# Performance work log

Hardware: AMD Instinct MI355X
Metric: run time of the kernel (lower is better)

The kernel has to match this reference:

```python
import jax, jax.numpy as jnp
import numpy as np

STRIDES = (8, 16, 32)
FMP = ((160, 160), (80, 80), (40, 40))
NUM_CLASSES = 80
TOPK = 1000
CONF_THRESH = 0.05
NMS_THRESH = 0.6
IMG_MAX = 1280.0
CLASS_OFFSET = 8192.0  # > any box coordinate, separates classes for batched NMS


def setup_inputs() -> dict:
    key = jax.random.key(0)
    ks = jax.random.split(key, 32)
    C = 256
    inp = {}
    for l, (h, w) in enumerate(FMP):
        inp[f'feat{l}'] = jax.random.normal(ks[l], (1, C, h, w), dtype=jnp.float32)
        inp[f'Wobj{l}'] = jax.random.normal(ks[3 + 6 * l + 0], (1, C), dtype=jnp.float32) * 0.05
        inp[f'bobj{l}'] = jnp.zeros((1,), dtype=jnp.float32)
        inp[f'Wcls{l}'] = jax.random.normal(ks[3 + 6 * l + 2], (NUM_CLASSES, C), dtype=jnp.float32) * 0.05
        inp[f'bcls{l}'] = jnp.zeros((NUM_CLASSES,), dtype=jnp.float32)
        inp[f'Wreg{l}'] = jax.random.normal(ks[3 + 6 * l + 4], (4, C), dtype=jnp.float32) * 0.05
        inp[f'breg{l}'] = jnp.zeros((4,), dtype=jnp.float32)
    return inp


def _level(feat, Wo, bo, Wc, bc, Wr, br, stride):
    x = feat[0]  # [C,H,W]
    H, W = x.shape[1], x.shape[2]
    def conv1x1(Wm, bv):
        # 1x1 conv == channel GEMM; output [H*W, O]
        return (jnp.einsum('oc,chw->hwo', Wm, x) + bv).reshape(H * W, -1)
    obj = conv1x1(Wo, bo)              # [M,1]
    cls = conv1x1(Wc, bc)              # [M,C]
    reg = jnp.exp(conv1x1(Wr, br)) * stride  # [M,4] (l,t,r,b)
    prob = jax.nn.sigmoid(obj) * jax.nn.sigmoid(cls)
    scores = prob.max(axis=-1)
    labels = prob.argmax(axis=-1)
    ay, ax = jnp.meshgrid(jnp.arange(H), jnp.arange(W), indexing='ij')
    anchors = (jnp.stack([ax, ay], axis=-1).astype(jnp.float32).reshape(-1, 2) + 0.5) * stride
    k = min(TOPK, H * W)
    scores, idx = jax.lax.top_k(scores, k)
    labels = labels[idx]
    reg = reg[idx]
    anchors = anchors[idx]
    boxes = jnp.concatenate([anchors - reg[:, :2], anchors + reg[:, 2:]], axis=-1)
    return scores, labels, boxes


def _batched_nms(boxes, scores, labels):
    N = boxes.shape[0]
    valid = scores >= CONF_THRESH
    # class-offset trick: per-class NMS == single NMS on disjoint offset boxes
    ob = boxes + labels.astype(boxes.dtype)[:, None] * CLASS_OFFSET
    order = jnp.argsort(-scores)
    b = ob[order]
    v = valid[order]
    x1, y1, x2, y2 = b[:, 0], b[:, 1], b[:, 2], b[:, 3]
    areas = (x2 - x1) * (y2 - y1)
    xx1 = jnp.maximum(x1[:, None], x1[None, :])
    yy1 = jnp.maximum(y1[:, None], y1[None, :])
    xx2 = jnp.minimum(x2[:, None], x2[None, :])
    yy2 = jnp.minimum(y2[:, None], y2[None, :])
    w = jnp.maximum(1e-10, xx2 - xx1)
    h = jnp.maximum(1e-10, yy2 - yy1)
    inter = w * h
    iou = inter / (areas[:, None] + areas[None, :] - inter + 1e-14)
    idxs = jnp.arange(N)
    def body(i, keep):
        sup = keep[i] & (iou[i] > NMS_THRESH) & (idxs > i)
        return keep & ~sup
    keep_sorted = jax.lax.fori_loop(0, N, body, v)
    keep = jnp.zeros(N, dtype=bool).at[order].set(keep_sorted)
    return keep


def reference(feat0, feat1, feat2,
              Wobj0, bobj0, Wcls0, bcls0, Wreg0, breg0,
              Wobj1, bobj1, Wcls1, bcls1, Wreg1, breg1,
              Wobj2, bobj2, Wcls2, bcls2, Wreg2, breg2):
    feats = (feat0, feat1, feat2)
    params = ((Wobj0, bobj0, Wcls0, bcls0, Wreg0, breg0),
              (Wobj1, bobj1, Wcls1, bcls1, Wreg1, breg1),
              (Wobj2, bobj2, Wcls2, bcls2, Wreg2, breg2))
    ss, ll, bb = [], [], []
    for l in range(3):
        s, lab, box = _level(feats[l], *params[l], STRIDES[l])
        ss.append(s); ll.append(lab); bb.append(box)
    scores = jnp.concatenate(ss)
    labels = jnp.concatenate(ll)
    boxes = jnp.concatenate(bb)
    keep = _batched_nms(boxes, scores, labels)
    bboxes = jnp.clip(boxes / IMG_MAX, 0.0, 1.0)
    return bboxes, scores, labels.astype(jnp.int32), keep
```

## Files before the change

### kernel.cpp

```cpp
#include <hip/hip_runtime.h>
#include <math.h>

#define NTOT   33600
#define NSEL   3000
#define CAND_CAP 8192
#define NWORDS 47
#define NROWS_PAD 3008
#define FCAP 4
#define NGRP 525
#define WPER 21760
#define NCH 17
#define NSLC 16

struct P21 {
  const float* feat[3];
  const float* Wobj[3];
  const float* bobj[3];
  const float* Wcls[3];
  const float* bcls[3];
  const float* Wreg[3];
  const float* breg[3];
};

__device__ __forceinline__ void level_of_block128(int b, int t, int& l, int& p, int& g,
                                                  int& HW, int& Wd, double& stride) {
  if (b < 200)      { l = 0; p = b * 128 + t;         g = p;          HW = 25600; Wd = 160; stride = 8.0;  }
  else if (b < 250) { l = 1; p = (b - 200) * 128 + t; g = 25600 + p;  HW = 6400;  Wd = 80;  stride = 16.0; }
  else              { l = 2; p = (b - 250) * 128 + t; g = 32000 + p;  HW = 1600;  Wd = 40;  stride = 32.0; }
}

__device__ __forceinline__ void level_of_group(int grp, int lane, int& l, int& p, int& g,
                                               int& HW, int& Wd, double& stride) {
  if (grp < 400)      { l = 0; p = grp * 64 + lane;         g = p;         HW = 25600; Wd = 160; stride = 8.0;  }
  else if (grp < 500) { l = 1; p = (grp - 400) * 64 + lane; g = 25600 + p; HW = 6400;  Wd = 80;  stride = 16.0; }
  else                { l = 2; p = (grp - 500) * 64 + lane; g = 32000 + p; HW = 1600;  Wd = 40;  stride = 32.0; }
}

__device__ __forceinline__ double sigmoid_d(double x) { return 1.0 / (1.0 + exp(-x)); }

__device__ __forceinline__ unsigned long long shfl64(unsigned long long v, int src) {
  unsigned lo = (unsigned)__shfl((int)(unsigned)(v & 0xFFFFFFFFull), src, 64);
  unsigned hi = (unsigned)__shfl((int)(unsigned)(v >> 32), src, 64);
  return (((unsigned long long)hi) << 32) | (unsigned long long)lo;
}

__global__ __launch_bounds__(256) void k_wconv(P21 P, double* __restrict__ W64) {
  int id = blockIdx.x * 256 + threadIdx.x;
  if (id >= 3 * WPER) return;
  int l = id / WPER, r = id - l * WPER;
  const float* src;
  if (r < 256)        src = P.Wobj[l] + r;
  else if (r < 1280)  src = P.Wreg[l] + (r - 256);
  else                src = P.Wcls[l] + (r - 1280);
  W64[id] = (double)(*src);
}

__global__ __launch_bounds__(128) void k_conv_chunk(P21 P, const double* __restrict__ W64,
    double* __restrict__ obj_t, double* __restrict__ reg_t,
    double* __restrict__ cmax, int* __restrict__ clab) {
  int l, p, g, HW, Wd; double stride;
  level_of_block128(blockIdx.x, threadIdx.x, l, p, g, HW, Wd, stride);
  if (p >= HW) return;
  const int ch = blockIdx.y;
  const float* __restrict__ fp = P.feat[l] + p;
  const double* __restrict__ Wl = W64 + l * WPER;

  if (ch == 0) {
    const double* __restrict__ Wo = Wl;
    const double* __restrict__ Wr = Wl + 256;
    double accO = (double)P.bobj[l][0];
    double accR[4];
#pragma unroll
    for (int j = 0; j < 4; j++) accR[j] = (double)P.breg[l][j];
    for (int c = 0; c < 256; c += 8) {
      double xc[8];
#pragma unroll
      for (int u = 0; u < 8; u++) xc[u] = (double)fp[(c + u) * HW];
#pragma unroll
      for (int u = 0; u < 8; u++) {
        accO = fma(Wo[c + u], xc[u], accO);
#pragma unroll
        for (int j = 0; j < 4; j++)
          accR[j] = fma(Wr[j * 256 + c + u], xc[u], accR[j]);
      }
    }
    obj_t[g] = accO;
#pragma unroll
    for (int j = 0; j < 4; j++) reg_t[4 * g + j] = accR[j];
  } else {
    const int base = (ch - 1) * 5;
    const double* __restrict__ Wc = Wl + 1280 + base * 256;
    const float* __restrict__ bcls = P.bcls[l];
    double a[5];
#pragma unroll
    for (int j = 0; j < 5; j++) a[j] = (double)bcls[base + j];
    for (int c = 0; c < 256; c += 8) {
      double xc[8];
#pragma unroll
      for (int u = 0; u < 8; u++) xc[u] = (double)fp[(c + u) * HW];
#pragma unroll
      for (int u = 0; u < 8; u++) {
#pragma unroll
        for (int j = 0; j < 5; j++)
          a[j] = fma(Wc[j * 256 + c + u], xc[u], a[j]);
      }
    }
    double maxv = a[0]; int lab = base;
#pragma unroll
    for (int j = 1; j < 5; j++) if (a[j] > maxv) { maxv = a[j]; lab = base + j; }
    cmax[(ch - 1) * NTOT + g] = maxv;
    clab[(ch - 1) * NTOT + g] = lab;
  }
}

__global__ __launch_bounds__(64) void k_combine(
    const double* __restrict__ obj_t, const double* __restrict__ reg_t,
    const double* __restrict__ cmax, const int* __restrict__ clab,
    double* __restrict__ score_d, int* __restrict__ label_d,
    double* __restrict__ box_d, unsigned* __restrict__ hist) {
  int l, p, g, HW, Wd; double stride;
  level_of_group(blockIdx.x, threadIdx.x, l, p, g, HW, Wd, stride);

  double maxv = cmax[g]; int lab = clab[g];
#pragma unroll
  for (int k = 1; k < NSLC; k++) {
    double v = cmax[k * NTOT + g];
    int lb = clab[k * NTOT + g];
    if (v > maxv) { maxv = v; lab = lb; }
  }
  double score = sigmoid_d(obj_t[g]) * sigmoid_d(maxv);
  int h = p / Wd, w = p - h * Wd;
  double ax = ((double)w + 0.5) * stride;
  double ay = ((double)h + 0.5) * stride;
  double e0 = exp(reg_t[4 * g + 0]) * stride;
  double e1 = exp(reg_t[4 * g + 1]) * stride;
  double e2 = exp(reg_t[4 * g + 2]) * stride;
  double e3 = exp(reg_t[4 * g + 3]) * stride;

  score_d[g] = score;
  label_d[g] = lab;
  box_d[4 * g + 0] = ax - e0;
  box_d[4 * g + 1] = ay - e1;
  box_d[4 * g + 2] = ax + e2;
  box_d[4 * g + 3] = ay + e3;

  unsigned key = __float_as_uint((float)score);
  atomicAdd(&hist[l * 65536 + (key >> 16)], 1u);
}

__global__ __launch_bounds__(256) void k_scan_a(const unsigned* __restrict__ hist,
                                                unsigned* __restrict__ csG) {
  const int lane = threadIdx.x & 63;
  const int row = blockIdx.x * 4 + (threadIdx.x >> 6);
  const uint4* hp = (const uint4*)(hist + row * 256);
  uint4 v = hp[lane];
  unsigned s = v.x + v.y + v.z + v.w;
#pragma unroll
  for (int off = 32; off > 0; off >>= 1) s += (unsigned)__shfl_down((int)s, off, 64);
  if (lane == 0) csG[row] = s;
}

__global__ __launch_bounds__(256) void k_scan_b(const unsigned* __restrict__ hist,
                                                const unsigned* __restrict__ csG,
                                                unsigned* __restrict__ cutB) {
  int l = blockIdx.x;
  __shared__ unsigned cs[256];
  __shared__ unsigned hb[256];
  __shared__ int s_chunk;
  __shared__ unsigned s_acc;
  int t = threadIdx.x;
  cs[t] = csG[l * 256 + t];
  __syncthreads();
  if (t == 0) {
    unsigned acc = 0; int chunk = 0;
    for (int tt = 255; tt >= 0; tt--) {
      if (acc + cs[tt] >= 1000u) { chunk = tt; break; }
      acc += cs[tt];
    }
    s_chunk = chunk; s_acc = acc;
  }
  __syncthreads();
  int chunk = s_chunk;
  hb[t] = hist[l * 65536 + chunk * 256 + t];
  __syncthreads();
  if (t == 0) {
    unsigned acc = s_acc;
    unsigned B = (unsigned)(chunk * 256);
    for (int b = 255; b >= 0; b--) {
      unsigned c = hb[b];
      if (acc + c >= 1000u) { B = (unsigned)(chunk * 256 + b); break; }
      acc += c;
    }
    cutB[l] = B;
  }
}

__global__ __launch_bounds__(64) void k_compact(const double* __restrict__ score_d,
    const unsigned* __restrict__ cutB, unsigned* __restrict__ cnt,
    double* __restrict__ cand_s, int* __restrict__ cand_g) {
  int l, p, g, HW, Wd; double stride;
  level_of_group(blockIdx.x, threadIdx.x, l, p, g, HW, Wd, stride);
  double sc = score_d[g];
  unsigned key = __float_as_uint((float)sc);
  if ((key >> 16) >= cutB[l]) {
    unsigned pos = atomicAdd(&cnt[l], 1u);
    if (pos < CAND_CAP) {
      cand_s[l * CAND_CAP + pos] = sc;
      cand_g[l * CAND_CAP + pos] = g;
    }
  }
}

__global__ __launch_bounds__(256) void k_rank(const double* __restrict__ cand_s,
    const int* __restrict__ cand_g, const unsigned* __restrict__ cnt,
    const int* __restrict__ label_d, const double* __restrict__ box_d,
    double* __restrict__ sel_s, int* __restrict__ sel_lab, double* __restrict__ sel_box) {
  const int l = blockIdx.y;
  const int M = (int)min(cnt[l], (unsigned)CAND_CAP);
  if (blockIdx.x * 4 >= M) return;
  const int q = blockIdx.x * 4 + (threadIdx.x >> 6);
  const int lane = threadIdx.x & 63;
  const bool active = (q < M);

  double s = 0.0; int g = 0;
  if (active) { s = cand_s[l * CAND_CAP + q]; g = cand_g[l * CAND_CAP + q]; }

  int r = 0;
  if (active) {
    for (int j = lane; j < M; j += 64) {
      double sj = cand_s[l * CAND_CAP + j];
      int gj = cand_g[l * CAND_CAP + j];
      r += (sj > s) || (sj == s && gj < g);
    }
  }
#pragma unroll
  for (int off = 32; off > 0; off >>= 1) r += __shfl_down(r, off, 64);

  if (active && lane == 0 && r < 1000) {
    int o = l * 1000 + r;
    sel_s[o] = s;
    sel_lab[o] = label_d[g];
    sel_box[4 * o + 0] = box_d[4 * g + 0];
    sel_box[4 * o + 1] = box_d[4 * g + 1];
    sel_box[4 * o + 2] = box_d[4 * g + 2];
    sel_box[4 * o + 3] = box_d[4 * g + 3];
  }
}

__global__ __launch_bounds__(256) void k_order(const double* __restrict__ sel_s,
                                               int* __restrict__ sortIdx) {
  const int i = blockIdx.x;
  const int t = threadIdx.x;
  const double s = sel_s[i];
  int r = 0;
  for (int j = t; j < NSEL; j += 256) {
    double sj = sel_s[j];
    r += (sj > s) || (sj == s && j < i);
  }
#pragma unroll
  for (int off = 32; off > 0; off >>= 1) r += __shfl_down(r, off, 64);
  __shared__ int wsum[4];
  if ((t & 63) == 0) wsum[t >> 6] = r;
  __syncthreads();
  if (t == 0) sortIdx[wsum[0] + wsum[1] + wsum[2] + wsum[3]] = i;
}

__global__ __launch_bounds__(256) void k_build(const double* __restrict__ sel_s,
    const int* __restrict__ sel_lab, const double* __restrict__ sel_box,
    const int* __restrict__ sortIdx, double* __restrict__ sbox, int* __restrict__ svalid) {
  int r = blockIdx.x * 256 + threadIdx.x;
  if (r >= NSEL) return;
  int i = sortIdx[r];
  double off = (double)sel_lab[i] * 8192.0;
  sbox[4 * r + 0] = sel_box[4 * i + 0] + off;
  sbox[4 * r + 1] = sel_box[4 * i + 1] + off;
  sbox[4 * r + 2] = sel_box[4 * i + 2] + off;
  sbox[4 * r + 3] = sel_box[4 * i + 3] + off;
  svalid[r] = (sel_s[i] >= 0.05) ? 1 : 0;
}

__global__ __launch_bounds__(256) void k_mask(const double* __restrict__ sbox,
    unsigned long long* __restrict__ denseG, unsigned long long* __restrict__ diagG,
    unsigned short* __restrict__ entG, int* __restrict__ cntGi) {
  const int w = blockIdx.x;
  const int rc = blockIdx.y;
  const int t = threadIdx.x, lane = t & 63, wk = t >> 6;
  const int rbase = rc * 64;
  if (w < rc) {
    int i = rbase + t;
    if (t < 64 && i < NSEL) denseG[(size_t)i * 48 + w] = 0ull;
    return;
  }
  __shared__ double rbox[256];
  {
    int idx = rbase * 4 + t;
    rbox[t] = (idx < NSEL * 4) ? sbox[idx] : 0.0;
  }
  const int j = w * 64 + lane;
  const bool jok = (j < NSEL);
  double bx1 = 0, by1 = 0, bx2 = 0, by2 = 0, arj = 0;
  if (jok) {
    bx1 = sbox[4 * j + 0]; by1 = sbox[4 * j + 1];
    bx2 = sbox[4 * j + 2]; by2 = sbox[4 * j + 3];
    arj = (bx2 - bx1) * (by2 - by1);
  }
  __syncthreads();
#pragma unroll
  for (int rr = 0; rr < 16; rr++) {
    const int ro = wk * 16 + rr;
    const int i = rbase + ro;
    if (i >= NSEL) break;
    double x1 = rbox[ro * 4 + 0], y1 = rbox[ro * 4 + 1];
    double x2 = rbox[ro * 4 + 2], y2 = rbox[ro * 4 + 3];
    double ar = (x2 - x1) * (y2 - y1);
    bool c = false;
    if (jok && j > i) {
      double xx1 = fmax(x1, bx1), yy1 = fmax(y1, by1);
      double xx2 = fmin(x2, bx2), yy2 = fmin(y2, by2);
      double ww = fmax(1e-10, xx2 - xx1);
      double hh = fmax(1e-10, yy2 - yy1);
      double inter = ww * hh;
      double iou = inter / (ar + arj - inter + 1e-14);
      c = iou > 0.6;
    }
    unsigned long long word = __ballot(c);
    if (lane == 0) {
      denseG[(size_t)i * 48 + w] = word;
      if (w == rc) diagG[i] = word;
      else if (word) {
        unsigned long long tt = word;
        while (tt) {
          int b = __builtin_ctzll(tt); tt &= tt - 1;
          int slot = atomicAdd(&cntGi[i], 1);
          if (slot < FCAP) entG[i * FCAP + slot] = (unsigned short)(w * 64 + b);
        }
      }
    }
  }
}

__global__ __launch_bounds__(256) void k_nms_scan(
    const unsigned long long* __restrict__ denseG, const unsigned long long* __restrict__ diagG,
    const unsigned short* __restrict__ entG, const int* __restrict__ cntGi,
    const int* __restrict__ svalid, const int* __restrict__ sortIdx,
    int* __restrict__ keepOrig) {
  __shared__ unsigned long long diagL[NROWS_PAD];
  __shared__ unsigned short entL[NROWS_PAD * FCAP];
  __shared__ unsigned short cntL[NROWS_PAD];
  __shared__ unsigned long long validL[48];
  __shared__ unsigned long long hasWL[48];
  const int t = threadIdx.x;
  const int lane = t & 63;

  for (int k = t; k < NSEL; k += 256) diagL[k] = diagG[k];
  for (int k = NSEL + t; k < NROWS_PAD; k += 256) diagL[k] = 0ull;
  uint2* e2 = (uint2*)entL; const uint2* eg2 = (const uint2*)entG;
  for (int k = t; k < NSEL; k += 256) e2[k] = eg2[k];
  for (int k = NSEL + t; k < NROWS_PAD; k += 256) { uint2 z; z.x = 0; z.y = 0; e2[k] = z; }
  for (int k = t; k < NSEL; k += 256) cntL[k] = (unsigned short)cntGi[k];
  for (int k = NSEL + t; k < NROWS_PAD; k += 256) cntL[k] = 0;
  for (int i0 = t; i0 < NROWS_PAD; i0 += 256) {
    bool f = (i0 < NSEL) && (svalid[i0] != 0);
    unsigned long long b = __ballot(f);
    if ((t & 63) == 0) validL[i0 >> 6] = b;
  }
  __syncthreads();
  if (t >= 64) return;

  for (int w = 0; w < NWORDS; w++) {
    int i = w * 64 + lane;
    bool f = (diagL[i] != 0ull) || (cntL[i] != 0);
    unsigned long long b = __ballot(f);
    if (lane == 0) hasWL[w] = b;
  }

  unsigned long long rem = 0ull;
  unsigned long long keep = 0ull;
  for (int w = 0; w < NWORDS; w++) {
    unsigned long long vw = validL[w];
    unsigned long long remw = shfl64(rem, w);
    unsigned long long win = vw & ~remw;
    unsigned long long work = hasWL[w];
    while (work) {
      int d = __builtin_ctzll(work); work &= work - 1;
      if ((win >> d) & 1ull) {
        int i = w * 64 + d;
        win &= ~diagL[i];
        int c = cntL[i];
        if (c > FCAP) {
          unsigned long long rowj = (lane < NWORDS) ? denseG[(size_t)i * 48 + lane] : 0ull;
          rem |= rowj;
        } else {
          for (int k = 0; k < c; k++) {
            int j = entL[i * FCAP + k];
            if ((j >> 6) == lane) rem |= 1ull << (j & 63);
          }
        }
      }
    }
    if (lane == w) keep = win;
  }
  if (lane < NWORDS) {
    for (int b = 0; b < 64; b++) {
      int j = lane * 64 + b;
      if (j < NSEL) keepOrig[sortIdx[j]] = (int)((keep >> b) & 1ull);
    }
  }
}

__global__ __launch_bounds__(256) void k_out(const double* __restrict__ sel_s,
    const int* __restrict__ sel_lab, const double* __restrict__ sel_box,
    const int* __restrict__ keepOrig, float* __restrict__ out) {
  int i = blockIdx.x * 256 + threadIdx.x;
  if (i >= NSEL) return;
#pragma unroll
  for (int c = 0; c < 4; c++) {
    double v = sel_box[4 * i + c] / 1280.0;
    v = fmin(fmax(v, 0.0), 1.0);
    out[4 * i + c] = (float)v;
  }
  out[12000 + i] = (float)sel_s[i];
  out[15000 + i] = (float)sel_lab[i];
  out[18000 + i] = keepOrig[i] ? 1.0f : 0.0f;
}

extern "C" void kernel_launch(void* const* d_in, const int* in_sizes, int n_in,
                              void* d_out, int out_size, void* d_ws, size_t ws_size,
                              hipStream_t stream) {
  P21 P;
  for (int l = 0; l < 3; l++) {
    P.feat[l] = (const float*)d_in[7 * l + 0];
    P.Wobj[l] = (const float*)d_in[7 * l + 1];
    P.bobj[l] = (const float*)d_in[7 * l + 2];
    P.Wcls[l] = (const float*)d_in[7 * l + 3];
    P.bcls[l] = (const float*)d_in[7 * l + 4];
    P.Wreg[l] = (const float*)d_in[7 * l + 5];
    P.breg[l] = (const float*)d_in[7 * l + 6];
  }

  char* ws = (char*)d_ws;
  size_t off = 0;
  auto alloc = [&](size_t bytes) -> char* {
    char* p = ws + off;
    off += (bytes + 15) & ~(size_t)15;
    return p;
  };
  double* score_d  = (double*)alloc((size_t)NTOT * 8);
  double* box_d    = (double*)alloc((size_t)NTOT * 4 * 8);
  int*    label_d  = (int*)   alloc((size_t)NTOT * 4);
  double* obj_t    = (double*)alloc((size_t)NTOT * 8);
  double* reg_t    = (double*)alloc((size_t)NTOT * 4 * 8);
  double* cmax     = (double*)alloc((size_t)NSLC * NTOT * 8);
  int*    clab     = (int*)   alloc((size_t)NSLC * NTOT * 4);
  double* W64      = (double*)alloc((size_t)3 * WPER * 8);
  double* sel_s    = (double*)alloc((size_t)NSEL * 8);
  double* sel_box  = (double*)alloc((size_t)NSEL * 4 * 8);
  int*    sel_lab  = (int*)   alloc((size_t)NSEL * 4);
  int*    sortIdx  = (int*)   alloc((size_t)NSEL * 4);
  double* sbox     = (double*)alloc((size_t)NSEL * 4 * 8);
  int*    svalid   = (int*)   alloc((size_t)NSEL * 4);
  int*    keepOrig = (int*)   alloc((size_t)NSEL * 4);
  double* cand_s   = (double*)alloc((size_t)3 * CAND_CAP * 8);
  int*    cand_g   = (int*)   alloc((size_t)3 * CAND_CAP * 4);
  unsigned long long* denseG = (unsigned long long*)alloc((size_t)NSEL * 48 * 8);
  unsigned long long* diagG  = (unsigned long long*)alloc((size_t)NSEL * 8);
  unsigned short*     entG   = (unsigned short*)alloc((size_t)NSEL * FCAP * 2);
  unsigned* hist   = (unsigned*)alloc((size_t)3 * 65536 * 4);
  unsigned* cnt    = (unsigned*)alloc(16);
  int*      cntGi  = (int*)   alloc((size_t)NSEL * 4);
  unsigned* cutB   = (unsigned*)alloc(16);
  unsigned* csG    = (unsigned*)alloc((size_t)768 * 4);

  hipMemsetAsync(hist, 0, (size_t)3 * 65536 * 4 + 16 + (size_t)NSEL * 4, stream);

  k_wconv   <<<(3 * WPER + 255) / 256, 256, 0, stream>>>(P, W64);
  dim3 cgrid(263, NCH, 1);
  k_conv_chunk<<<cgrid, 128, 0, stream>>>(P, W64, obj_t, reg_t, cmax, clab);
  k_combine <<<NGRP, 64, 0, stream>>>(obj_t, reg_t, cmax, clab, score_d, label_d, box_d, hist);
  k_scan_a  <<<192, 256, 0, stream>>>(hist, csG);
  k_scan_b  <<<3, 256, 0, stream>>>(hist, csG, cutB);
  k_compact <<<NGRP, 64, 0, stream>>>(score_d, cutB, cnt, cand_s, cand_g);
  dim3 rgrid(CAND_CAP / 4, 3, 1);
  k_rank    <<<rgrid, 256, 0, stream>>>(cand_s, cand_g, cnt, label_d, box_d,
                                        sel_s, sel_lab, sel_box);
  k_order   <<<NSEL, 256, 0, stream>>>(sel_s, sortIdx);
  k_build   <<<(NSEL + 255) / 256, 256, 0, stream>>>(sel_s, sel_lab, sel_box, sortIdx, sbox, svalid);
  dim3 mgrid(NWORDS, NWORDS, 1);
  k_mask    <<<mgrid, 256, 0, stream>>>(sbox, denseG, diagG, entG, cntGi);
  k_nms_scan<<<1, 256, 0, stream>>>(denseG, diagG, entG, cntGi, svalid, sortIdx, keepOrig);
  k_out     <<<(NSEL + 255) / 256, 256, 0, stream>>>(sel_s, sel_lab, sel_box, keepOrig, (float*)d_out);
}
```

Baseline: 307.0 us.

## Register-block conv over two pixels and eight classes, fuse build into order, triangular mask grid

The 1x1-conv kernel now computes two adjacent pixels per thread with float2 loads and eight classes per chunk instead of five, which halves the block count and reuses each fp64 weight load across two pixels. The k_build kernel is folded into k_order so the sorted boxes are written directly. The mask kernel launches only the upper-triangular tiles, and the lower tiles are zeroed by a memset. This trades higher register pressure in the conv for fewer weight loads and fewer launches, and adds a small serial loop per mask block to decode its tile index.

```diff
diff --git a/kernel.cpp b/kernel.cpp
--- a/kernel.cpp
+++ b/kernel.cpp
@@ -9,8 +9,8 @@
 #define FCAP 4
 #define NGRP 525
 #define WPER 21760
-#define NCH 17
-#define NSLC 16
+#define NSLC 10
+#define NTRI 1128
 
 struct P21 {
   const float* feat[3];
@@ -22,13 +22,6 @@
   const float* breg[3];
 };
 
-__device__ __forceinline__ void level_of_block128(int b, int t, int& l, int& p, int& g,
-                                                  int& HW, int& Wd, double& stride) {
-  if (b < 200)      { l = 0; p = b * 128 + t;         g = p;          HW = 25600; Wd = 160; stride = 8.0;  }
-  else if (b < 250) { l = 1; p = (b - 200) * 128 + t; g = 25600 + p;  HW = 6400;  Wd = 80;  stride = 16.0; }
-  else              { l = 2; p = (b - 250) * 128 + t; g = 32000 + p;  HW = 1600;  Wd = 40;  stride = 32.0; }
-}
-
 __device__ __forceinline__ void level_of_group(int grp, int lane, int& l, int& p, int& g,
                                                int& HW, int& Wd, double& stride) {
   if (grp < 400)      { l = 0; p = grp * 64 + lane;         g = p;         HW = 25600; Wd = 160; stride = 8.0;  }
@@ -58,8 +51,11 @@
 __global__ __launch_bounds__(128) void k_conv_chunk(P21 P, const double* __restrict__ W64,
     double* __restrict__ obj_t, double* __restrict__ reg_t,
     double* __restrict__ cmax, int* __restrict__ clab) {
-  int l, p, g, HW, Wd; double stride;
-  level_of_block128(blockIdx.x, threadIdx.x, l, p, g, HW, Wd, stride);
+  const int b = blockIdx.x, t = threadIdx.x;
+  int l, p, g, HW;
+  if (b < 100)      { l = 0; p = b * 256 + 2 * t;         g = p;         HW = 25600; }
+  else if (b < 125) { l = 1; p = (b - 100) * 256 + 2 * t; g = 25600 + p; HW = 6400;  }
+  else              { l = 2; p = (b - 125) * 256 + 2 * t; g = 32000 + p; HW = 1600;  }
   if (p >= HW) return;
   const int ch = blockIdx.y;
   const float* __restrict__ fp = P.feat[l] + p;
@@ -68,48 +64,62 @@
   if (ch == 0) {
     const double* __restrict__ Wo = Wl;
     const double* __restrict__ Wr = Wl + 256;
-    double accO = (double)P.bobj[l][0];
-    double accR[4];
-#pragma unroll
-    for (int j = 0; j < 4; j++) accR[j] = (double)P.breg[l][j];
+    double o0 = (double)P.bobj[l][0], o1 = o0;
+    double r0[4], r1[4];
+#pragma unroll
+    for (int j = 0; j < 4; j++) { r0[j] = (double)P.breg[l][j]; r1[j] = r0[j]; }
     for (int c = 0; c < 256; c += 8) {
-      double xc[8];
-#pragma unroll
-      for (int u = 0; u < 8; u++) xc[u] = (double)fp[(c + u) * HW];
+      double x0[8], x1[8];
 #pragma unroll
       for (int u = 0; u < 8; u++) {
-        accO = fma(Wo[c + u], xc[u], accO);
-#pragma unroll
-        for (int j = 0; j < 4; j++)
-          accR[j] = fma(Wr[j * 256 + c + u], xc[u], accR[j]);
-      }
-    }
-    obj_t[g] = accO;
-#pragma unroll
-    for (int j = 0; j < 4; j++) reg_t[4 * g + j] = accR[j];
+        float2 v = *(const float2*)(fp + (c + u) * HW);
+        x0[u] = (double)v.x; x1[u] = (double)v.y;
+      }
+#pragma unroll
+      for (int u = 0; u < 8; u++) {
+        double w = Wo[c + u];
+        o0 = fma(w, x0[u], o0); o1 = fma(w, x1[u], o1);
+#pragma unroll
+        for (int j = 0; j < 4; j++) {
+          double wr = Wr[j * 256 + c + u];
+          r0[j] = fma(wr, x0[u], r0[j]); r1[j] = fma(wr, x1[u], r1[j]);
+        }
+      }
+    }
+    obj_t[g] = o0; obj_t[g + 1] = o1;
+#pragma unroll
+    for (int j = 0; j < 4; j++) { reg_t[4 * g + j] = r0[j]; reg_t[4 * g + 4 + j] = r1[j]; }
   } else {
-    const int base = (ch - 1) * 5;
+    const int base = (ch - 1) * 8;
     const double* __restrict__ Wc = Wl + 1280 + base * 256;
     const float* __restrict__ bcls = P.bcls[l];
-    double a[5];
-#pragma unroll
-    for (int j = 0; j < 5; j++) a[j] = (double)bcls[base + j];
+    double a0[8], a1[8];
+#pragma unroll
+    for (int j = 0; j < 8; j++) { a0[j] = (double)bcls[base + j]; a1[j] = a0[j]; }
     for (int c = 0; c < 256; c += 8) {
-      double xc[8];
-#pragma unroll
-      for (int u = 0; u < 8; u++) xc[u] = (double)fp[(c + u) * HW];
+      double x0[8], x1[8];
 #pragma unroll
       for (int u = 0; u < 8; u++) {
-#pragma unroll
-        for (int j = 0; j < 5; j++)
-          a[j] = fma(Wc[j * 256 + c + u], xc[u], a[j]);
-      }
-    }
-    double maxv = a[0]; int lab = base;
-#pragma unroll
-    for (int j = 1; j < 5; j++) if (a[j] > maxv) { maxv = a[j]; lab = base + j; }
-    cmax[(ch - 1) * NTOT + g] = maxv;
-    clab[(ch - 1) * NTOT + g] = lab;
+        float2 v = *(const float2*)(fp + (c + u) * HW);
+        x0[u] = (double)v.x; x1[u] = (double)v.y;
+      }
+#pragma unroll
+      for (int u = 0; u < 8; u++) {
+#pragma unroll
+        for (int j = 0; j < 8; j++) {
+          double w = Wc[j * 256 + c + u];
+          a0[j] = fma(w, x0[u], a0[j]); a1[j] = fma(w, x1[u], a1[j]);
+        }
+      }
+    }
+    double m0 = a0[0], m1 = a1[0]; int l0 = base, l1 = base;
+#pragma unroll
+    for (int j = 1; j < 8; j++) {
+      if (a0[j] > m0) { m0 = a0[j]; l0 = base + j; }
+      if (a1[j] > m1) { m1 = a1[j]; l1 = base + j; }
+    }
+    cmax[(ch - 1) * NTOT + g] = m0; cmax[(ch - 1) * NTOT + g + 1] = m1;
+    clab[(ch - 1) * NTOT + g] = l0; clab[(ch - 1) * NTOT + g + 1] = l1;
   }
 }
 
@@ -248,7 +258,8 @@
 }
 
 __global__ __launch_bounds__(256) void k_order(const double* __restrict__ sel_s,
-                                               int* __restrict__ sortIdx) {
+    const int* __restrict__ sel_lab, const double* __restrict__ sel_box,
+    int* __restrict__ sortIdx, double* __restrict__ sbox, int* __restrict__ svalid) {
   const int i = blockIdx.x;
   const int t = threadIdx.x;
   const double s = sel_s[i];
@@ -262,35 +273,26 @@
   __shared__ int wsum[4];
   if ((t & 63) == 0) wsum[t >> 6] = r;
   __syncthreads();
-  if (t == 0) sortIdx[wsum[0] + wsum[1] + wsum[2] + wsum[3]] = i;
-}
-
-__global__ __launch_bounds__(256) void k_build(const double* __restrict__ sel_s,
-    const int* __restrict__ sel_lab, const double* __restrict__ sel_box,
-    const int* __restrict__ sortIdx, double* __restrict__ sbox, int* __restrict__ svalid) {
-  int r = blockIdx.x * 256 + threadIdx.x;
-  if (r >= NSEL) return;
-  int i = sortIdx[r];
-  double off = (double)sel_lab[i] * 8192.0;
-  sbox[4 * r + 0] = sel_box[4 * i + 0] + off;
-  sbox[4 * r + 1] = sel_box[4 * i + 1] + off;
-  sbox[4 * r + 2] = sel_box[4 * i + 2] + off;
-  sbox[4 * r + 3] = sel_box[4 * i + 3] + off;
-  svalid[r] = (sel_s[i] >= 0.05) ? 1 : 0;
+  if (t == 0) {
+    int rr = wsum[0] + wsum[1] + wsum[2] + wsum[3];
+    sortIdx[rr] = i;
+    double off = (double)sel_lab[i] * 8192.0;
+    sbox[4 * rr + 0] = sel_box[4 * i + 0] + off;
+    sbox[4 * rr + 1] = sel_box[4 * i + 1] + off;
+    sbox[4 * rr + 2] = sel_box[4 * i + 2] + off;
+    sbox[4 * rr + 3] = sel_box[4 * i + 3] + off;
+    svalid[rr] = (s >= 0.05) ? 1 : 0;
+  }
 }
 
 __global__ __launch_bounds__(256) void k_mask(const double* __restrict__ sbox,
     unsigned long long* __restrict__ denseG, unsigned long long* __restrict__ diagG,
     unsigned short* __restrict__ entG, int* __restrict__ cntGi) {
-  const int w = blockIdx.x;
-  const int rc = blockIdx.y;
+  int k = blockIdx.x, rc = 0;
+  while (k >= NWORDS - rc) { k -= NWORDS - rc; rc++; }
+  const int w = rc + k;
   const int t = threadIdx.x, lane = t & 63, wk = t >> 6;
   const int rbase = rc * 64;
-  if (w < rc) {
-    int i = rbase + t;
-    if (t < 64 && i < NSEL) denseG[(size_t)i * 48 + w] = 0ull;
-    return;
-  }
   __shared__ double rbox[256];
   {
     int idx = rbase * 4 + t;
@@ -472,9 +474,10 @@
   unsigned* csG    = (unsigned*)alloc((size_t)768 * 4);
 
   hipMemsetAsync(hist, 0, (size_t)3 * 65536 * 4 + 16 + (size_t)NSEL * 4, stream);
+  hipMemsetAsync(denseG, 0, (size_t)NSEL * 48 * 8, stream);
 
   k_wconv   <<<(3 * WPER + 255) / 256, 256, 0, stream>>>(P, W64);
-  dim3 cgrid(263, NCH, 1);
+  dim3 cgrid(132, 11, 1);
   k_conv_chunk<<<cgrid, 128, 0, stream>>>(P, W64, obj_t, reg_t, cmax, clab);
   k_combine <<<NGRP, 64, 0, stream>>>(obj_t, reg_t, cmax, clab, score_d, label_d, box_d, hist);
   k_scan_a  <<<192, 256, 0, stream>>>(hist, csG);
@@ -483,10 +486,8 @@
   dim3 rgrid(CAND_CAP / 4, 3, 1);
   k_rank    <<<rgrid, 256, 0, stream>>>(cand_s, cand_g, cnt, label_d, box_d,
                                         sel_s, sel_lab, sel_box);
-  k_order   <<<NSEL, 256, 0, stream>>>(sel_s, sortIdx);
-  k_build   <<<(NSEL + 255) / 256, 256, 0, stream>>>(sel_s, sel_lab, sel_box, sortIdx, sbox, svalid);
-  dim3 mgrid(NWORDS, NWORDS, 1);
-  k_mask    <<<mgrid, 256, 0, stream>>>(sbox, denseG, diagG, entG, cntGi);
+  k_order   <<<NSEL, 256, 0, stream>>>(sel_s, sel_lab, sel_box, sortIdx, sbox, svalid);
+  k_mask    <<<NTRI, 256, 0, stream>>>(sbox, denseG, diagG, entG, cntGi);
   k_nms_scan<<<1, 256, 0, stream>>>(denseG, diagG, entG, cntGi, svalid, sortIdx, keepOrig);
   k_out     <<<(NSEL + 255) / 256, 256, 0, stream>>>(sel_s, sel_lab, sel_box, keepOrig, (float*)d_out);
 }
```

Result: faster. 277.6 us (-9.6%).
